# Kernel tuning notes

Hardware: AMD Instinct MI355X
Metric: run time of the kernel (lower is better)

The kernel has to match this reference:

```python
import jax, jax.numpy as jnp
import numpy as np


def setup_inputs() -> dict:
    key = jax.random.key(0)
    k1, k2 = jax.random.split(key)
    B, Q, K, H = 8, 2048, 2048, 128
    out_state = jax.random.normal(k1, (B, Q, H), dtype=jnp.float32)
    history = jax.random.normal(k2, (B, K, H), dtype=jnp.float32)
    return {"out_state": out_state, "history": history}


def reference(out_state, history):
    # tanh pre-activation on queries
    q = jnp.tanh(out_state)                              # [B, Q, H]
    # unscaled QK^T scores
    scores = jnp.einsum("bqh,bkh->bqk", q, history)      # [B, Q, K]
    probs = jax.nn.softmax(scores, axis=2)               # softmax over keys
    attn = jnp.einsum("bqk,bkh->bqh", probs, history)    # [B, Q, H]
    return attn
```

## Files before the change

kernel.cpp:

```cpp
#include <hip/hip_runtime.h>
#include <math.h>


typedef _Float16 half8  __attribute__((ext_vector_type(8)));
typedef _Float16 half4  __attribute__((ext_vector_type(4)));
typedef __fp16   fp16x2 __attribute__((ext_vector_type(2)));
typedef float    f32x4  __attribute__((ext_vector_type(4)));
typedef float    f32x16 __attribute__((ext_vector_type(16)));

#define QQ 2048
#define KK 2048
#define HH 128
#define QBM 128
#define BN 64
#define NTILES 32
#define L2E 1.44269504f

#define KH_HALVES      ((size_t)8 * KK * HH)
#define PREP_BYTES     (KH_HALVES * 4)
#define OSPLIT_BYTES   ((size_t)128 * QBM * HH * 2)
#define MLSPLIT_FLOATS ((size_t)128 * QBM)

union U32H { unsigned int u; _Float16 h[2]; };
union U64H { unsigned long long u; _Float16 h[4]; };
union H2I  { fp16x2 h; int i; };
union I4H8 { int i[4]; half8 h; };

typedef __attribute__((address_space(1))) const void gvoid;
typedef __attribute__((address_space(3))) void lvoid;

#define WAITVM4 asm volatile("s_waitcnt vmcnt(4)" ::: "memory")
#define WAITVM0 asm volatile("s_waitcnt vmcnt(0)" ::: "memory")
static __device__ __forceinline__ void wgbar() {
    asm volatile("" ::: "memory");
    __builtin_amdgcn_s_barrier();
    asm volatile("" ::: "memory");
}

__launch_bounds__(256)
__global__ void attn_prep_k(const float* __restrict__ history,
                            _Float16* __restrict__ wsh) {
    __shared__ __align__(16) _Float16 Ks[BN * HH];
    __shared__ __align__(16) _Float16 Vt[HH * BN];

    const int tid = threadIdx.x;
    const int bid = blockIdx.x;
    const int b   = bid >> 5;
    const int kt  = bid & 31;

    const float* hb = history + ((size_t)b * KK + (size_t)kt * BN) * HH;
    const int r0 = tid >> 5;
    const int c4 = (tid & 31) * 4;
    #pragma unroll
    for (int j = 0; j < 8; ++j) {
        const int k = r0 + 8 * j;
        const float4 g = *(const float4*)(hb + (size_t)k * HH + c4);
        half4 hv;
        hv[0] = (_Float16)g.x; hv[1] = (_Float16)g.y;
        hv[2] = (_Float16)g.z; hv[3] = (_Float16)g.w;
        *(half4*)&Ks[k * HH + (c4 ^ ((k & 7) << 3))] = hv;
    }
    __syncthreads();

    {
        const int h0  = 2 * (tid & 63);
        const int n0t = (tid >> 6) * 16;
        half8 ra0, ra1, rb0, rb1;
        #pragma unroll
        for (int i = 0; i < 8; ++i) {
            const int n = n0t + i;
            U32H t; t.u = *(const unsigned int*)&Ks[n * HH + (h0 ^ ((n & 7) << 3))];
            ra0[i] = t.h[0]; rb0[i] = t.h[1];
        }
        #pragma unroll
        for (int i = 8; i < 16; ++i) {
            const int n = n0t + i;
            U32H t; t.u = *(const unsigned int*)&Ks[n * HH + (h0 ^ ((n & 7) << 3))];
            ra1[i - 8] = t.h[0]; rb1[i - 8] = t.h[1];
        }
        const int th0 = (h0 & 7) << 3;
        const int th1 = ((h0 + 1) & 7) << 3;
        *(half8*)&Vt[(h0    ) * BN + ((n0t    ) ^ th0)] = ra0;
        *(half8*)&Vt[(h0    ) * BN + ((n0t + 8) ^ th0)] = ra1;
        *(half8*)&Vt[(h0 + 1) * BN + ((n0t    ) ^ th1)] = rb0;
        *(half8*)&Vt[(h0 + 1) * BN + ((n0t + 8) ^ th1)] = rb1;
    }
    __syncthreads();

    _Float16* kdst = wsh + ((size_t)b * KK + (size_t)kt * BN) * HH;
    _Float16* vdst = wsh + KH_HALVES + ((size_t)(b * NTILES + kt)) * (HH * BN);
    const f32x4* ksrc = (const f32x4*)Ks;
    const f32x4* vsrc = (const f32x4*)Vt;
    #pragma unroll
    for (int i = 0; i < 4; ++i) {
        ((f32x4*)kdst)[i * 256 + tid] = ksrc[i * 256 + tid];
        ((f32x4*)vdst)[i * 256 + tid] = vsrc[i * 256 + tid];
    }
}

__launch_bounds__(256, 2)
__global__ void attn_main_k(const float* __restrict__ out_state,
                            const _Float16* __restrict__ wsh,
                            float* __restrict__ out,
                            char* __restrict__ wsb,
                            int splits) {
    __shared__ __align__(16) _Float16 KsL[2][BN * HH];
    __shared__ __align__(16) _Float16 VtL[2][HH * BN];

    const int tid  = threadIdx.x;
    const int wave = tid >> 6;
    const int lane = tid & 63;
    const int l31  = lane & 31;
    const int hi   = lane >> 5;
    const int swzk = (lane & 7) << 3;

    const int nwg  = gridDim.x;
    const int cpx  = nwg >> 3;
    const int work = (blockIdx.x & 7) * cpx + (blockIdx.x >> 3);
    const int s    = work >> 7;
    const int r128 = work & 127;
    const int b    = r128 >> 4;
    const int qb   = r128 & 15;
    const int q    = qb * QBM + wave * 32 + l31;

    const int kt0 = (NTILES * s) / splits;
    const int kt1 = (NTILES * (s + 1)) / splits;

    const _Float16* khb = wsh + (size_t)b * KK * HH;
    const _Float16* vtb = wsh + KH_HALVES + (size_t)b * NTILES * (HH * BN);

    auto issueK = [&](int t, int pb) {
        const char* g = (const char*)(khb + (size_t)t * (BN * HH));
        #pragma unroll
        for (int c = 0; c < 4; ++c) {
            const int off = (c * 4 + wave) * 1024 + lane * 16;
            __builtin_amdgcn_global_load_lds((gvoid*)(g + off),
                                             (lvoid*)((char*)KsL[pb] + off), 16, 0, 0);
        }
    };
    auto issueV = [&](int t, int pb) {
        const char* g = (const char*)(vtb + (size_t)t * (HH * BN));
        #pragma unroll
        for (int c = 0; c < 4; ++c) {
            const int off = (c * 4 + wave) * 1024 + lane * 16;
            __builtin_amdgcn_global_load_lds((gvoid*)(g + off),
                                             (lvoid*)((char*)VtL[pb] + off), 16, 0, 0);
        }
    };

    float4 qa[16];
    {
        const float* qrow = out_state + ((size_t)b * QQ + q) * HH;
        #pragma unroll
        for (int hs = 0; hs < 8; ++hs) {
            qa[2 * hs]     = *(const float4*)(qrow + hs * 16 + hi * 8);
            qa[2 * hs + 1] = *(const float4*)(qrow + hs * 16 + hi * 8 + 4);
        }
    }
    issueK(kt0, 0);
    issueV(kt0, 0);

    auto th = [](float x) {
        const float e = __builtin_amdgcn_exp2f(x * (2.0f * L2E));
        return 1.0f - 2.0f * __builtin_amdgcn_rcpf(e + 1.0f);
    };
    half8 qf[8];
    #pragma unroll
    for (int hs = 0; hs < 8; ++hs) {
        const float4 a = qa[2 * hs], c = qa[2 * hs + 1];
        qf[hs][0] = (_Float16)th(a.x); qf[hs][1] = (_Float16)th(a.y);
        qf[hs][2] = (_Float16)th(a.z); qf[hs][3] = (_Float16)th(a.w);
        qf[hs][4] = (_Float16)th(c.x); qf[hs][5] = (_Float16)th(c.y);
        qf[hs][6] = (_Float16)th(c.z); qf[hs][7] = (_Float16)th(c.w);
    }

    f32x16 O[4];
    #pragma unroll
    for (int i = 0; i < 4; ++i)
        #pragma unroll
        for (int r = 0; r < 16; ++r) O[i][r] = 0.f;
    float Osum = 0.f;
    float rmax = -3.0e38f;

    for (int kt = kt0; kt < kt1; ++kt) {
        const int  pb   = kt & 1;
        const bool more = (kt + 1 < kt1);

        WAITVM4;
        wgbar();
        if (more) issueK(kt + 1, pb ^ 1);

        f32x16 S0, S1;
        #pragma unroll
        for (int r = 0; r < 16; ++r) { S0[r] = 0.f; S1[r] = 0.f; }
        __builtin_amdgcn_s_setprio(1);
        #pragma unroll
        for (int hs = 0; hs < 8; ++hs) {
            const int col = (hs * 16 + hi * 8) ^ swzk;
            const half8 k0 = *(const half8*)&KsL[pb][l31 * 128 + col];
            const half8 k1 = *(const half8*)&KsL[pb][(l31 + 32) * 128 + col];
            S0 = __builtin_amdgcn_mfma_f32_32x32x16_f16(k0, qf[hs], S0, 0, 0, 0);
            S1 = __builtin_amdgcn_mfma_f32_32x32x16_f16(k1, qf[hs], S1, 0, 0, 0);
        }
        __builtin_amdgcn_s_setprio(0);

        float tmax = S0[0];
        #pragma unroll
        for (int r = 1; r < 16; ++r) tmax = fmaxf(tmax, S0[r]);
        #pragma unroll
        for (int r = 0; r < 16; ++r) tmax = fmaxf(tmax, S1[r]);
        tmax = fmaxf(tmax, __shfl_xor(tmax, 32, 64));

        if (!__all(tmax <= rmax)) {
            const float nm    = fmaxf(rmax, tmax);
            const float alpha = __builtin_amdgcn_exp2f((rmax - nm) * L2E);
            rmax = nm;
            #pragma unroll
            for (int i = 0; i < 4; ++i) O[i] *= alpha;
            Osum *= alpha;
        }

        #pragma unroll
        for (int r = 0; r < 16; ++r) S0[r] = __builtin_amdgcn_exp2f((S0[r] - rmax) * L2E);
        #pragma unroll
        for (int r = 0; r < 16; ++r) S1[r] = __builtin_amdgcn_exp2f((S1[r] - rmax) * L2E);

        float ls = 0.f;
        #pragma unroll
        for (int r = 0; r < 16; ++r) ls += S0[r] + S1[r];
        Osum += ls + __shfl_xor(ls, 32, 64);

        int d0[8], d1[8];
        #pragma unroll
        for (int M = 0; M < 8; ++M) {
            const int r0 = (M & 3) * 4;
            H2I u0, u1;
            if (M < 4) {
                u0.h = __builtin_amdgcn_cvt_pkrtz(S0[r0], S0[r0 + 1]);
                u1.h = __builtin_amdgcn_cvt_pkrtz(S0[r0 + 2], S0[r0 + 3]);
            } else {
                u0.h = __builtin_amdgcn_cvt_pkrtz(S1[r0], S1[r0 + 1]);
                u1.h = __builtin_amdgcn_cvt_pkrtz(S1[r0 + 2], S1[r0 + 3]);
            }
            d0[M] = u0.i; d1[M] = u1.i;
        }

        if (more) { WAITVM4; } else { WAITVM0; }
        wgbar();
        if (more) issueV(kt + 1, pb ^ 1);

        __builtin_amdgcn_s_setprio(1);
        #pragma unroll
        for (int ns = 0; ns < 4; ++ns) {
            const int x  = d0[2 * ns],     x2 = d1[2 * ns];
            const int y  = d0[2 * ns + 1], y2 = d1[2 * ns + 1];
            const int px  = __shfl_xor(x, 32, 64),  px2 = __shfl_xor(x2, 32, 64);
            const int py  = __shfl_xor(y, 32, 64),  py2 = __shfl_xor(y2, 32, 64);
            I4H8 bf;
            bf.i[0] = hi ? py  : x;
            bf.i[1] = hi ? py2 : x2;
            bf.i[2] = hi ? y   : px;
            bf.i[3] = hi ? y2  : px2;
            #pragma unroll
            for (int ht = 0; ht < 4; ++ht) {
                const half8 vf = *(const half8*)
                    &VtL[pb][(ht * 32 + l31) * 64 + ((ns * 16 + hi * 8) ^ swzk)];
                O[ht] = __builtin_amdgcn_mfma_f32_32x32x16_f16(vf, bf.h, O[ht], 0, 0, 0);
            }
        }
        __builtin_amdgcn_s_setprio(0);
    }

    if (splits == 1) {
        const float inv = 1.0f / Osum;
        float* orow = out + ((size_t)b * QQ + q) * HH;
        #pragma unroll
        for (int ht = 0; ht < 4; ++ht)
            #pragma unroll
            for (int m = 0; m < 4; ++m) {
                f32x4 v;
                v[0] = O[ht][4 * m]     * inv; v[1] = O[ht][4 * m + 1] * inv;
                v[2] = O[ht][4 * m + 2] * inv; v[3] = O[ht][4 * m + 3] * inv;
                *(f32x4*)&orow[ht * 32 + 8 * m + 4 * hi] = v;
            }
    } else {
        const float inv = 1.0f / Osum;
        _Float16* oh = (_Float16*)(wsb + PREP_BYTES)
                     + ((size_t)(s * 128 + r128) * QBM + wave * 32 + l31) * HH;
        #pragma unroll
        for (int ht = 0; ht < 4; ++ht)
            #pragma unroll
            for (int m = 0; m < 4; ++m) {
                half4 hv;
                hv[0] = (_Float16)(O[ht][4 * m]     * inv);
                hv[1] = (_Float16)(O[ht][4 * m + 1] * inv);
                hv[2] = (_Float16)(O[ht][4 * m + 2] * inv);
                hv[3] = (_Float16)(O[ht][4 * m + 3] * inv);
                *(half4*)&oh[ht * 32 + 8 * m + 4 * hi] = hv;
            }
        if (!hi) {
            float* wm = (float*)(wsb + PREP_BYTES + (size_t)splits * OSPLIT_BYTES);
            const size_t idx = (size_t)(s * 128 + r128) * QBM + wave * 32 + l31;
            wm[idx] = rmax;
            wm[(size_t)splits * MLSPLIT_FLOATS + idx] = Osum;
        }
    }
}

template<int SPL>
__launch_bounds__(256)
__global__ void attn_combine_k(const char* __restrict__ wsb,
                               float* __restrict__ out) {
    const int idx = blockIdx.x * 256 + threadIdx.x;
    const int h4  = idx & 31;
    const int q   = (idx >> 5) & 2047;
    const int b   = idx >> 16;
    const int blk = b * 16 + (q >> 7);
    const int qr  = q & 127;

    const _Float16* oh = (const _Float16*)(wsb + PREP_BYTES);
    const float* wm = (const float*)(wsb + PREP_BYTES + (size_t)SPL * OSPLIT_BYTES);
    const float* wl = wm + (size_t)SPL * MLSPLIT_FLOATS;

    float ms[SPL];
    float M = -3.0e38f;
    #pragma unroll
    for (int s = 0; s < SPL; ++s) {
        ms[s] = wm[(size_t)(s * 128 + blk) * QBM + qr];
        M = fmaxf(M, ms[s]);
    }
    float denom = 0.f;
    float v0 = 0.f, v1 = 0.f, v2 = 0.f, v3 = 0.f;
    #pragma unroll
    for (int s = 0; s < SPL; ++s) {
        const float wgt = exp2f((ms[s] - M) * L2E) * wl[(size_t)(s * 128 + blk) * QBM + qr];
        denom += wgt;
        U64H t;
        t.u = *(const unsigned long long*)&oh[((size_t)(s * 128 + blk) * QBM + qr) * HH
                                              + 4 * h4];
        v0 += wgt * (float)t.h[0];
        v1 += wgt * (float)t.h[1];
        v2 += wgt * (float)t.h[2];
        v3 += wgt * (float)t.h[3];
    }
    const float inv = 1.0f / denom;
    f32x4 r; r[0] = v0 * inv; r[1] = v1 * inv; r[2] = v2 * inv; r[3] = v3 * inv;
    *(f32x4*)&out[((size_t)(b * QQ + q)) * HH + 4 * h4] = r;
}

extern "C" void kernel_launch(void* const* d_in, const int* in_sizes, int n_in,
                              void* d_out, int out_size, void* d_ws, size_t ws_size,
                              hipStream_t stream) {
    const float* out_state = (const float*)d_in[0];
    const float* history   = (const float*)d_in[1];
    float* out = (float*)d_out;
    char* wsb  = (char*)d_ws;

    const size_t need4 = PREP_BYTES + 4 * OSPLIT_BYTES + 4 * 2 * MLSPLIT_FLOATS * 4;
    const size_t need3 = PREP_BYTES + 3 * OSPLIT_BYTES + 3 * 2 * MLSPLIT_FLOATS * 4;
    const int splits = (ws_size >= need4) ? 4 : (ws_size >= need3) ? 3 : 1;

    attn_prep_k<<<dim3(256), dim3(256), 0, stream>>>(history, (_Float16*)wsb);
    attn_main_k<<<dim3(128 * splits), dim3(256), 0, stream>>>(out_state, (const _Float16*)wsb,
                                                              out, wsb, splits);
    if (splits == 4)
        attn_combine_k<4><<<dim3(2048), dim3(256), 0, stream>>>(wsb, out);
    else if (splits == 3)
        attn_combine_k<3><<<dim3(2048), dim3(256), 0, stream>>>(wsb, out);
}
```

Measured before the change: 108.0 us.

## Single-buffer V tile for 3 blocks/CU, add 6-way split, dot2 row sums

Drops the V tile in shared memory from double to single buffering, with an extra barrier before loading the next V tile. This cuts LDS per block so three blocks can fit per CU, and launch bounds are raised to 3. A 6-way K split is added when the workspace allows, so more blocks are in flight. The row-sum is computed from the packed fp16 probabilities with fdot2, and the max reduction is restructured as a tree. The cost is less overlap of V loads with compute, tighter register limits, and more combine work, plus a slightly different rounding of the softmax denominator.

```diff
diff --git a/kernel.cpp b/kernel.cpp
--- a/kernel.cpp
+++ b/kernel.cpp
@@ -98,14 +98,14 @@
     }
 }
 
-__launch_bounds__(256, 2)
+__launch_bounds__(256, 3)
 __global__ void attn_main_k(const float* __restrict__ out_state,
                             const _Float16* __restrict__ wsh,
                             float* __restrict__ out,
                             char* __restrict__ wsb,
                             int splits) {
     __shared__ __align__(16) _Float16 KsL[2][BN * HH];
-    __shared__ __align__(16) _Float16 VtL[2][HH * BN];
+    __shared__ __align__(16) _Float16 VtL[HH * BN];
 
     const int tid  = threadIdx.x;
     const int wave = tid >> 6;
@@ -138,13 +138,13 @@
                                              (lvoid*)((char*)KsL[pb] + off), 16, 0, 0);
         }
     };
-    auto issueV = [&](int t, int pb) {
+    auto issueV = [&](int t) {
         const char* g = (const char*)(vtb + (size_t)t * (HH * BN));
         #pragma unroll
         for (int c = 0; c < 4; ++c) {
             const int off = (c * 4 + wave) * 1024 + lane * 16;
             __builtin_amdgcn_global_load_lds((gvoid*)(g + off),
-                                             (lvoid*)((char*)VtL[pb] + off), 16, 0, 0);
+                                             (lvoid*)((char*)VtL + off), 16, 0, 0);
         }
     };
 
@@ -158,7 +158,7 @@
         }
     }
     issueK(kt0, 0);
-    issueV(kt0, 0);
+    issueV(kt0);
 
     auto th = [](float x) {
         const float e = __builtin_amdgcn_exp2f(x * (2.0f * L2E));
@@ -182,8 +182,10 @@
     float Osum = 0.f;
     float rmax = -3.0e38f;
 
+    const H2I one2 = { fp16x2{(__fp16)1.f, (__fp16)1.f} };
+
     for (int kt = kt0; kt < kt1; ++kt) {
-        const int  pb   = kt & 1;
+        const int  pb   = (kt - kt0) & 1;
         const bool more = (kt + 1 < kt1);
 
         WAITVM4;
@@ -204,11 +206,11 @@
         }
         __builtin_amdgcn_s_setprio(0);
 
-        float tmax = S0[0];
-        #pragma unroll
-        for (int r = 1; r < 16; ++r) tmax = fmaxf(tmax, S0[r]);
-        #pragma unroll
-        for (int r = 0; r < 16; ++r) tmax = fmaxf(tmax, S1[r]);
+        float tmax = fmaxf(S0[14], S0[15]);
+        #pragma unroll
+        for (int r = 0; r < 14; r += 2) tmax = fmaxf(fmaxf(S0[r], S0[r + 1]), tmax);
+        #pragma unroll
+        for (int r = 0; r < 16; r += 2) tmax = fmaxf(fmaxf(S1[r], S1[r + 1]), tmax);
         tmax = fmaxf(tmax, __shfl_xor(tmax, 32, 64));
 
         if (!__all(tmax <= rmax)) {
@@ -224,11 +226,6 @@
         for (int r = 0; r < 16; ++r) S0[r] = __builtin_amdgcn_exp2f((S0[r] - rmax) * L2E);
         #pragma unroll
         for (int r = 0; r < 16; ++r) S1[r] = __builtin_amdgcn_exp2f((S1[r] - rmax) * L2E);
-
-        float ls = 0.f;
-        #pragma unroll
-        for (int r = 0; r < 16; ++r) ls += S0[r] + S1[r];
-        Osum += ls + __shfl_xor(ls, 32, 64);
 
         int d0[8], d1[8];
         #pragma unroll
@@ -245,9 +242,23 @@
             d0[M] = u0.i; d1[M] = u1.i;
         }
 
+        {
+            float ls = 0.f;
+            #pragma unroll
+            for (int M = 0; M < 8; ++M) {
+                H2I a; a.i = d0[M];
+                ls = __builtin_amdgcn_fdot2(a.h, one2.h, ls, false);
+            }
+            #pragma unroll
+            for (int M = 0; M < 8; ++M) {
+                H2I a; a.i = d1[M];
+                ls = __builtin_amdgcn_fdot2(a.h, one2.h, ls, false);
+            }
+            Osum += ls + __shfl_xor(ls, 32, 64);
+        }
+
         if (more) { WAITVM4; } else { WAITVM0; }
         wgbar();
-        if (more) issueV(kt + 1, pb ^ 1);
 
         __builtin_amdgcn_s_setprio(1);
         #pragma unroll
@@ -264,11 +275,14 @@
             #pragma unroll
             for (int ht = 0; ht < 4; ++ht) {
                 const half8 vf = *(const half8*)
-                    &VtL[pb][(ht * 32 + l31) * 64 + ((ns * 16 + hi * 8) ^ swzk)];
+                    &VtL[(ht * 32 + l31) * 64 + ((ns * 16 + hi * 8) ^ swzk)];
                 O[ht] = __builtin_amdgcn_mfma_f32_32x32x16_f16(vf, bf.h, O[ht], 0, 0, 0);
             }
         }
         __builtin_amdgcn_s_setprio(0);
+
+        wgbar();
+        if (more) issueV(kt + 1);
     }
 
     if (splits == 1) {
@@ -356,14 +370,19 @@
     float* out = (float*)d_out;
     char* wsb  = (char*)d_ws;
 
+    const size_t need6 = PREP_BYTES + 6 * OSPLIT_BYTES + 6 * 2 * MLSPLIT_FLOATS * 4;
     const size_t need4 = PREP_BYTES + 4 * OSPLIT_BYTES + 4 * 2 * MLSPLIT_FLOATS * 4;
     const size_t need3 = PREP_BYTES + 3 * OSPLIT_BYTES + 3 * 2 * MLSPLIT_FLOATS * 4;
-    const int splits = (ws_size >= need4) ? 4 : (ws_size >= need3) ? 3 : 1;
+    const int splits = (ws_size >= need6) ? 6
+                     : (ws_size >= need4) ? 4
+                     : (ws_size >= need3) ? 3 : 1;
 
     attn_prep_k<<<dim3(256), dim3(256), 0, stream>>>(history, (_Float16*)wsb);
     attn_main_k<<<dim3(128 * splits), dim3(256), 0, stream>>>(out_state, (const _Float16*)wsb,
                                                               out, wsb, splits);
-    if (splits == 4)
+    if (splits == 6)
+        attn_combine_k<6><<<dim3(2048), dim3(256), 0, stream>>>(wsb, out);
+    else if (splits == 4)
         attn_combine_k<4><<<dim3(2048), dim3(256), 0, stream>>>(wsb, out);
     else if (splits == 3)
         attn_combine_k<3><<<dim3(2048), dim3(256), 0, stream>>>(wsb, out);
```

After: 134.7 us. 24.8% more time.
